# Optimization experiments

Hardware: AMD Instinct MI355X
Metric: run time of the kernel (lower is better)

Reference implementation:

```python
import jax, jax.numpy as jnp
import numpy as np
from jax import lax

V, E, H = 32000, 512, 1024  # vocab, embedding_dim, hidden_dim
S, B, T = 50, 64, 10        # src len, batch, max decode steps
SOS = 0


def setup_inputs() -> dict:
    key = jax.random.key(0)
    ks = jax.random.split(key, 16)
    sc = 0.02
    n = jax.random.normal
    return {
        "enc_out": n(ks[0], (S, B, 2 * H), jnp.float32),
        "hidden": n(ks[1], (1, B, H), jnp.float32),
        "target": jax.random.randint(ks[2], (B, T), 0, V),
        "emb": n(ks[3], (V, E), jnp.float32) * sc,
        "w_ih": n(ks[4], (3 * H, E), jnp.float32) * sc,
        "w_hh": n(ks[5], (3 * H, H), jnp.float32) * sc,
        "b_ih": n(ks[6], (3 * H,), jnp.float32) * sc,
        "b_hh": n(ks[7], (3 * H,), jnp.float32) * sc,
        "wa_w": n(ks[8], (H, H), jnp.float32) * sc,
        "wa_b": n(ks[9], (H,), jnp.float32) * sc,
        "ua_w": n(ks[10], (H, 2 * H), jnp.float32) * sc,
        "ua_b": n(ks[11], (H,), jnp.float32) * sc,
        "va_w": n(ks[12], (1, H), jnp.float32) * sc,
        "va_b": n(ks[13], (1,), jnp.float32) * sc,
    }


def reference(enc_out, hidden, target, emb, w_ih, w_hh, b_ih, b_hh,
              wa_w, wa_b, ua_w, ua_b, va_w, va_b):
    b, t = target.shape

    def gru_cell(x, h):
        gi = x @ w_ih.T + b_ih          # [B, 3H]
        gh = h @ w_hh.T + b_hh          # [B, 3H]
        ir, iz, inn = jnp.split(gi, 3, axis=-1)
        hr, hz, hn = jnp.split(gh, 3, axis=-1)
        r = jax.nn.sigmoid(ir + hr)
        z = jax.nn.sigmoid(iz + hz)
        nng = jnp.tanh(inn + r * hn)
        return (1.0 - z) * nng + z * h

    # teacher-forced decoder inputs: [SOS, target[:, :-1]] -> [T, B]
    dec_in = jnp.concatenate(
        [jnp.full((b, 1), SOS, dtype=target.dtype), target[:, : t - 1]], axis=1)
    xs = emb[dec_in].transpose(1, 0, 2)  # [T, B, E] (dropout is identity in eval)

    def step(h, x):
        h2 = gru_cell(x, h)
        return h2, h2

    h_last, hs = lax.scan(step, hidden[0], xs)   # hs: [T, B, H]

    keys = enc_out.transpose(1, 0, 2)            # [B, S, 2H]
    uk = keys @ ua_w.T + ua_b                    # [B, S, H]
    wq = hs @ wa_w.T + wa_b                      # [T, B, H]
    # additive (Bahdanau) scores: [T, B, S]
    scores = (jnp.tanh(wq[:, :, None, :] + uk[None]) @ va_w.T + va_b)[..., 0]
    weights = jax.nn.softmax(scores, axis=-1)    # over source positions
    context = jnp.einsum('tbs,bsd->btd', weights, keys)  # [B, T, 2H]
    out = jax.nn.log_softmax(context, axis=-1)   # [B, T, 2H]
    return out, h_last
```

## Files before the change

### kernel.cpp

```cpp
#include <hip/hip_runtime.h>
#include <math.h>

#define VOCAB 32000
#define E_DIM 512
#define H_DIM 1024
#define S_LEN 50
#define B_SZ 64
#define T_LEN 10
#define H3 (3 * H_DIM)
#define D2H (2 * H_DIM)

typedef __attribute__((ext_vector_type(8))) short short8;
typedef __attribute__((ext_vector_type(4))) float floatx4;

__device__ __forceinline__ ushort f2b(float f) {
    union { float f; uint32_t u; } x; x.f = f;
    uint32_t r = (x.u + 0x7fff + ((x.u >> 16) & 1)) >> 16;
    return (ushort)r;
}
__device__ __forceinline__ float b2f(ushort u) {
    union { float f; uint32_t u; } x; x.u = ((uint32_t)u) << 16;
    return x.f;
}
__device__ __forceinline__ float fast_sigmoid(float x) {
    x = fminf(fmaxf(x, -30.f), 30.f);
    return 1.f / (1.f + __expf(-x));
}
__device__ __forceinline__ float fast_tanh(float x) {
    x = fminf(fmaxf(x, -15.f), 15.f);
    float e = __expf(2.f * x);
    return (e - 1.f) / (e + 1.f);
}

#define PB0 1536
#define PB1 (PB0 + 3072)
#define PB2 (PB1 + 2048)
#define PB3 (PB2 + 1024)
#define PB4 (PB3 + 3200)
#define PB5 (PB4 + 640)
#define PB6 (PB5 + 64)

__device__ __forceinline__ void cvt_chunk(const float* src, ushort* dst, int i) {
    float4 v = ((const float4*)src)[i];
    ushort4 o;
    o.x = f2b(v.x); o.y = f2b(v.y); o.z = f2b(v.z); o.w = f2b(v.w);
    ((ushort4*)dst)[i] = o;
}

__global__ __launch_bounds__(256) void prep(
    const float* __restrict__ w_ih, ushort* __restrict__ w_ihb,
    const float* __restrict__ w_hh, ushort* __restrict__ w_hhb,
    const float* __restrict__ ua_w, ushort* __restrict__ ua_wb,
    const float* __restrict__ wa_w, ushort* __restrict__ wa_wb,
    const float* __restrict__ enc_out, ushort* __restrict__ keysb,
    const int* __restrict__ target, const float* __restrict__ emb,
    ushort* __restrict__ Xb,
    const float* __restrict__ hidden, ushort* __restrict__ hb0,
    int* __restrict__ bar) {
    int bid = blockIdx.x, tid = threadIdx.x;
    if (bid == 0) {
        for (int i = tid; i < 4096; i += 256)
            __hip_atomic_store(&bar[i], 0, __ATOMIC_RELAXED, __HIP_MEMORY_SCOPE_AGENT);
    }
    if (bid < PB0) {
        cvt_chunk(w_ih, w_ihb, bid * 256 + tid);
    } else if (bid < PB1) {
        cvt_chunk(w_hh, w_hhb, (bid - PB0) * 256 + tid);
    } else if (bid < PB2) {
        cvt_chunk(ua_w, ua_wb, (bid - PB1) * 256 + tid);
    } else if (bid < PB3) {
        cvt_chunk(wa_w, wa_wb, (bid - PB2) * 256 + tid);
    } else if (bid < PB4) {
        int bs = bid - PB3;
        int b = bs / S_LEN, s = bs % S_LEN;
        const float* src = enc_out + ((size_t)s * B_SZ + b) * D2H;
        ushort* dst = keysb + (size_t)bs * D2H;
#pragma unroll
        for (int p = 0; p < 2; ++p) {
            int i = tid + p * 256;
            float4 v = ((const float4*)src)[i];
            ushort4 o;
            o.x = f2b(v.x); o.y = f2b(v.y); o.z = f2b(v.z); o.w = f2b(v.w);
            ((ushort4*)dst)[i] = o;
        }
    } else if (bid < PB5) {
        int m = bid - PB4;
        int t = m / B_SZ, b = m % B_SZ;
        int idx = (t == 0) ? 0 : target[b * T_LEN + (t - 1)];
        if (tid < 128) {
            const float* src = emb + (size_t)idx * E_DIM;
            float4 v = ((const float4*)src)[tid];
            ushort4 o;
            o.x = f2b(v.x); o.y = f2b(v.y); o.z = f2b(v.z); o.w = f2b(v.w);
            ((ushort4*)(Xb + (size_t)m * E_DIM))[tid] = o;
        }
    } else {
        cvt_chunk(hidden, hb0, (bid - PB5) * 256 + tid);
    }
}

struct GemmArgs {
    const ushort* A; const ushort* W; const float* bias;
    float* Cf; ushort* C16;
    int M, N, K, nbn, nblk;
};

__global__ __launch_bounds__(256) void gemm_bf16(GemmArgs g0, GemmArgs g1) {
    const bool first = (int)blockIdx.x < g0.nblk;
    GemmArgs g = first ? g0 : g1;
    const int bid = first ? blockIdx.x : (blockIdx.x - g0.nblk);

    __shared__ ushort As[64 * 72];
    __shared__ ushort Bs[128 * 72];

    const int tid = threadIdx.x;
    const int w = tid >> 6, lane = tid & 63;
    const int lm = lane & 15, q = lane >> 4;
    const int wm = w >> 1, wn = w & 1;
    const int n0 = (bid % g.nbn) * 128;
    const int m0 = (bid / g.nbn) * 64;
    const int K = g.K;

    floatx4 acc[2][4];
#pragma unroll
    for (int i = 0; i < 2; ++i)
#pragma unroll
        for (int j = 0; j < 4; ++j)
            acc[i][j] = (floatx4){0.f, 0.f, 0.f, 0.f};

    short8 ar[2], br[4];
    auto load_tiles = [&](int k0) {
#pragma unroll
        for (int p = 0; p < 2; ++p) {
            int c = tid + p * 256;
            ar[p] = *(const short8*)&g.A[(size_t)(m0 + (c >> 3)) * K + k0 + (c & 7) * 8];
        }
#pragma unroll
        for (int p = 0; p < 4; ++p) {
            int c = tid + p * 256;
            br[p] = *(const short8*)&g.W[(size_t)(n0 + (c >> 3)) * K + k0 + (c & 7) * 8];
        }
    };

    load_tiles(0);
    for (int k0 = 0; k0 < K; k0 += 64) {
#pragma unroll
        for (int p = 0; p < 2; ++p) {
            int c = tid + p * 256;
            *(short8*)&As[(c >> 3) * 72 + (c & 7) * 8] = ar[p];
        }
#pragma unroll
        for (int p = 0; p < 4; ++p) {
            int c = tid + p * 256;
            *(short8*)&Bs[(c >> 3) * 72 + (c & 7) * 8] = br[p];
        }
        __syncthreads();
        if (k0 + 64 < K) load_tiles(k0 + 64);

#pragma unroll
        for (int kk = 0; kk < 2; ++kk) {
            short8 af[2], bf[4];
#pragma unroll
            for (int i = 0; i < 2; ++i)
                af[i] = *(const short8*)&As[(wm * 32 + i * 16 + lm) * 72 + kk * 32 + q * 8];
#pragma unroll
            for (int j = 0; j < 4; ++j)
                bf[j] = *(const short8*)&Bs[(wn * 64 + j * 16 + lm) * 72 + kk * 32 + q * 8];
#pragma unroll
            for (int i = 0; i < 2; ++i)
#pragma unroll
                for (int j = 0; j < 4; ++j)
                    acc[i][j] = __builtin_amdgcn_mfma_f32_16x16x32_bf16(af[i], bf[j], acc[i][j], 0, 0, 0);
        }
        __syncthreads();
    }

    float bv[4];
#pragma unroll
    for (int j = 0; j < 4; ++j)
        bv[j] = g.bias[n0 + wn * 64 + j * 16 + lm];
#pragma unroll
    for (int i = 0; i < 2; ++i) {
#pragma unroll
        for (int j = 0; j < 4; ++j) {
            int col = n0 + wn * 64 + j * 16 + lm;
#pragma unroll
            for (int r = 0; r < 4; ++r) {
                int row = m0 + wm * 32 + i * 16 + q * 4 + r;
                float v = acc[i][j][r] + bv[j];
                if (g.C16) g.C16[(size_t)row * g.N + col] = f2b(v);
                else       g.Cf[(size_t)row * g.N + col] = v;
            }
        }
    }
}

#define GRU_BLOCKS 64
#define WS_STRIDE 1032

__device__ __forceinline__ void grid_barrier(int* __restrict__ bar, int t, int bid) {
    __syncthreads();
    if (threadIdx.x == 0) {
        __builtin_amdgcn_fence(__ATOMIC_RELEASE, "agent");
        int g = bid & 7;
        int sub = __hip_atomic_fetch_add(&bar[(t * 8 + g) * 32], 1,
                                         __ATOMIC_RELAXED, __HIP_MEMORY_SCOPE_AGENT);
        if (sub == 7) {
            int m = __hip_atomic_fetch_add(&bar[2560 + t * 32], 1,
                                           __ATOMIC_RELAXED, __HIP_MEMORY_SCOPE_AGENT);
            if (m == 7)
                __hip_atomic_store(&bar[3040], t + 1,
                                   __ATOMIC_RELAXED, __HIP_MEMORY_SCOPE_AGENT);
        }
        while (__hip_atomic_load(&bar[3040], __ATOMIC_RELAXED,
                                 __HIP_MEMORY_SCOPE_AGENT) <= t)
            __builtin_amdgcn_s_sleep(1);
        __builtin_amdgcn_fence(__ATOMIC_ACQUIRE, "agent");
    }
    __syncthreads();
}

__global__ __launch_bounds__(256, 1) void gru_persistent(
    const ushort* __restrict__ w_hhb, const float* __restrict__ bhh,
    const float* __restrict__ GI, const float* __restrict__ hidden,
    const ushort* __restrict__ hb0, ushort* __restrict__ hsb,
    float* __restrict__ outTail, int* __restrict__ bar) {
    __shared__ ushort Ws[48 * WS_STRIDE];
    const int tid = threadIdx.x;
    const int w = tid >> 6, lane = tid & 63;
    const int lm = lane & 15, q = lane >> 4;
    const int bid = blockIdx.x;
    const int j0 = bid * 16;
    const int j = j0 + lm;

#pragma unroll
    for (int p = 0; p < 24; ++p) {
        int c = tid + p * 256;
        int row = c >> 7, off = c & 127;
        int grow = (row >> 4) * H_DIM + j0 + (row & 15);
        *(short8*)&Ws[row * WS_STRIDE + off * 8] =
            *(const short8*)&w_hhb[(size_t)grow * H_DIM + off * 8];
    }

    const float bhr = bhh[j], bhz = bhh[H_DIM + j], bhn = bhh[2 * H_DIM + j];

    float hf[4];
#pragma unroll
    for (int r = 0; r < 4; ++r)
        hf[r] = hidden[(size_t)(w * 16 + q * 4 + r) * H_DIM + j];

    float ir[4], iz[4], inn[4];
#pragma unroll
    for (int r = 0; r < 4; ++r) {
        const float* gi = GI + (size_t)(w * 16 + q * 4 + r) * H3 + j;
        ir[r] = gi[0]; iz[r] = gi[H_DIM]; inn[r] = gi[2 * H_DIM];
    }

    __syncthreads();

    for (int t = 0; t < T_LEN; ++t) {
        const ushort* hin = (t == 0) ? hb0 : hsb + (size_t)(t - 1) * B_SZ * H_DIM;
        ushort* hout = hsb + (size_t)t * B_SZ * H_DIM;
        const ushort* arow = hin + (size_t)(w * 16 + lm) * H_DIM + q * 8;

        short8 hreg[32];
#pragma unroll
        for (int c = 0; c < 32; ++c)
            hreg[c] = *(const short8*)&arow[c * 32];

        floatx4 accr = {0.f, 0.f, 0.f, 0.f};
        floatx4 accz = {0.f, 0.f, 0.f, 0.f};
        floatx4 accn = {0.f, 0.f, 0.f, 0.f};

#pragma unroll
        for (int it = 0; it < 8; ++it) {
#pragma unroll
            for (int kk = 0; kk < 4; ++kk) {
                const short8 af = hreg[it * 4 + kk];
                const int ko = it * 128 + kk * 32 + q * 8;
                short8 b0 = *(const short8*)&Ws[(lm) * WS_STRIDE + ko];
                short8 b1 = *(const short8*)&Ws[(16 + lm) * WS_STRIDE + ko];
                short8 b2 = *(const short8*)&Ws[(32 + lm) * WS_STRIDE + ko];
                accr = __builtin_amdgcn_mfma_f32_16x16x32_bf16(af, b0, accr, 0, 0, 0);
                accz = __builtin_amdgcn_mfma_f32_16x16x32_bf16(af, b1, accz, 0, 0, 0);
                accn = __builtin_amdgcn_mfma_f32_16x16x32_bf16(af, b2, accn, 0, 0, 0);
            }
        }

#pragma unroll
        for (int r = 0; r < 4; ++r) {
            int b = w * 16 + q * 4 + r;
            float rg = fast_sigmoid(ir[r] + accr[r] + bhr);
            float z  = fast_sigmoid(iz[r] + accz[r] + bhz);
            float ng = fast_tanh(inn[r] + rg * (accn[r] + bhn));
            float hnew = (1.f - z) * ng + z * hf[r];
            hf[r] = hnew;
            size_t hi = (size_t)b * H_DIM + j;
            hout[hi] = f2b(hnew);
            if (t == T_LEN - 1) outTail[hi] = hnew;
        }

        if (t < T_LEN - 1) {
#pragma unroll
            for (int r = 0; r < 4; ++r) {
                const float* gi = GI + (size_t)((t + 1) * B_SZ + w * 16 + q * 4 + r) * H3 + j;
                ir[r] = gi[0]; iz[r] = gi[H_DIM]; inn[r] = gi[2 * H_DIM];
            }
            grid_barrier(bar, t, bid);
        }
    }
}

__global__ __launch_bounds__(256) void attn_ctx(
    const ushort* __restrict__ WQ16, const ushort* __restrict__ UK16,
    const float* __restrict__ va_w, const float* __restrict__ va_b,
    const ushort* __restrict__ keysb, float* __restrict__ out) {
    __shared__ float wq_s[H_DIM];
    __shared__ float va_s[H_DIM];
    __shared__ float sc[S_LEN];
    __shared__ float wred[4];
    __shared__ float sred[4];
    const int bt = blockIdx.x;
    const int t = bt >> 6, b = bt & 63;
    const int tid = threadIdx.x;
    const int wave = tid >> 6, lane = tid & 63;

    for (int hh = tid; hh < H_DIM; hh += 256) {
        wq_s[hh] = b2f(WQ16[(size_t)(t * B_SZ + b) * H_DIM + hh]);
        va_s[hh] = va_w[hh];
    }
    __syncthreads();

    for (int s = wave; s < S_LEN; s += 4) {
        const ushort* uk = UK16 + ((size_t)b * S_LEN + s) * H_DIM + lane * 16;
        short8 u0 = *(const short8*)&uk[0];
        short8 u1 = *(const short8*)&uk[8];
        float acc = 0.f;
        const int h0 = lane * 16;
#pragma unroll
        for (int i = 0; i < 8; ++i)
            acc += fast_tanh(wq_s[h0 + i] + b2f((ushort)u0[i])) * va_s[h0 + i];
#pragma unroll
        for (int i = 0; i < 8; ++i)
            acc += fast_tanh(wq_s[h0 + 8 + i] + b2f((ushort)u1[i])) * va_s[h0 + 8 + i];
        for (int off = 32; off > 0; off >>= 1) acc += __shfl_down(acc, off);
        if (lane == 0) sc[s] = acc + va_b[0];
    }
    __syncthreads();

    if (tid < 64) {
        float v = (tid < S_LEN) ? sc[tid] : -INFINITY;
        float m = v;
        for (int off = 32; off > 0; off >>= 1) m = fmaxf(m, __shfl_down(m, off));
        m = __shfl(m, 0);
        float e = (tid < S_LEN) ? __expf(v - m) : 0.f;
        float sum = e;
        for (int off = 32; off > 0; off >>= 1) sum += __shfl_down(sum, off);
        sum = __shfl(sum, 0);
        if (tid < S_LEN) sc[tid] = e / sum;
    }
    __syncthreads();

    float c[8];
#pragma unroll
    for (int i = 0; i < 8; ++i) c[i] = 0.f;
    const ushort* kb = keysb + (size_t)b * S_LEN * D2H + tid * 8;
    for (int s = 0; s < S_LEN; ++s) {
        float ws = sc[s];
        short8 kv = *(const short8*)&kb[(size_t)s * D2H];
#pragma unroll
        for (int i = 0; i < 8; ++i) c[i] += ws * b2f((ushort)kv[i]);
    }

    float m = c[0];
#pragma unroll
    for (int i = 1; i < 8; ++i) m = fmaxf(m, c[i]);
    for (int off = 32; off > 0; off >>= 1) m = fmaxf(m, __shfl_down(m, off));
    if (lane == 0) wred[wave] = m;
    __syncthreads();
    if (tid == 0) wred[0] = fmaxf(fmaxf(wred[0], wred[1]), fmaxf(wred[2], wred[3]));
    __syncthreads();
    m = wred[0];
    float sum = 0.f;
#pragma unroll
    for (int i = 0; i < 8; ++i) sum += __expf(c[i] - m);
    for (int off = 32; off > 0; off >>= 1) sum += __shfl_down(sum, off);
    if (lane == 0) sred[wave] = sum;
    __syncthreads();
    if (tid == 0) sred[0] = sred[0] + sred[1] + sred[2] + sred[3];
    __syncthreads();
    float lse = m + __logf(sred[0]);

    float* o = out + ((size_t)b * T_LEN + t) * D2H + tid * 8;
#pragma unroll
    for (int i = 0; i < 8; ++i) o[i] = c[i] - lse;
}

extern "C" void kernel_launch(void* const* d_in, const int* in_sizes, int n_in,
                              void* d_out, int out_size, void* d_ws, size_t ws_size,
                              hipStream_t stream) {
    const float* enc_out = (const float*)d_in[0];
    const float* hidden  = (const float*)d_in[1];
    const int*   target  = (const int*)d_in[2];
    const float* emb     = (const float*)d_in[3];
    const float* w_ih    = (const float*)d_in[4];
    const float* w_hh    = (const float*)d_in[5];
    const float* b_ih    = (const float*)d_in[6];
    const float* b_hh    = (const float*)d_in[7];
    const float* wa_w    = (const float*)d_in[8];
    const float* wa_b    = (const float*)d_in[9];
    const float* ua_w    = (const float*)d_in[10];
    const float* ua_b    = (const float*)d_in[11];
    const float* va_w    = (const float*)d_in[12];
    const float* va_b    = (const float*)d_in[13];
    float* out = (float*)d_out;

    const int TB = T_LEN * B_SZ;
    const int BS = B_SZ * S_LEN;

    char* p = (char*)d_ws;
    int*    bar   = (int*)p;    p += 4096 * 4;
    float*  GI    = (float*)p;  p += (size_t)TB * H3 * 4;
    p = (char*)(((uintptr_t)p + 255) & ~(uintptr_t)255);
    ushort* keysb = (ushort*)p; p += (size_t)BS * D2H * 2;
    ushort* Xb    = (ushort*)p; p += (size_t)TB * E_DIM * 2;
    ushort* w_ihb = (ushort*)p; p += (size_t)H3 * E_DIM * 2;
    ushort* w_hhb = (ushort*)p; p += (size_t)H3 * H_DIM * 2;
    ushort* ua_wb = (ushort*)p; p += (size_t)H_DIM * D2H * 2;
    ushort* wa_wb = (ushort*)p; p += (size_t)H_DIM * H_DIM * 2;
    ushort* hb0   = (ushort*)p; p += (size_t)B_SZ * H_DIM * 2;
    ushort* hsb   = (ushort*)p; p += (size_t)TB * H_DIM * 2;
    ushort* UK16  = (ushort*)p; p += (size_t)BS * H_DIM * 2;
    ushort* WQ16  = (ushort*)p; p += (size_t)TB * H_DIM * 2;

    prep<<<PB6, 256, 0, stream>>>(w_ih, w_ihb, w_hh, w_hhb, ua_w, ua_wb, wa_w, wa_wb,
                                  enc_out, keysb, target, emb, Xb, hidden, hb0, bar);

    GemmArgs guk = { keysb, ua_wb, ua_b, nullptr, UK16,
                     BS, H_DIM, D2H, H_DIM / 128, (BS / 64) * (H_DIM / 128) };
    GemmArgs ggi = { Xb, w_ihb, b_ih, GI, nullptr,
                     TB, H3, E_DIM, H3 / 128, (TB / 64) * (H3 / 128) };
    gemm_bf16<<<guk.nblk + ggi.nblk, 256, 0, stream>>>(guk, ggi);

    float* outTail = out + (size_t)B_SZ * T_LEN * D2H;
    gru_persistent<<<GRU_BLOCKS, 256, 0, stream>>>(w_hhb, b_hh, GI, hidden,
                                                   hb0, hsb, outTail, bar);

    GemmArgs gwq = { hsb, wa_wb, wa_b, nullptr, WQ16,
                     TB, H_DIM, H_DIM, H_DIM / 128, (TB / 64) * (H_DIM / 128) };
    gemm_bf16<<<gwq.nblk, 256, 0, stream>>>(gwq, gwq);

    attn_ctx<<<B_SZ * T_LEN, 256, 0, stream>>>(WQ16, UK16, va_w, va_b, keysb, out);
}
```

Baseline: 332.9 us.

## Replace grid-barrier fences with system-scope atomics and cache-bypassing hidden-state loads

Measured after the change: 309.2 us. -7.1%, faster.

```diff
diff --git a/kernel.cpp b/kernel.cpp
--- a/kernel.cpp
+++ b/kernel.cpp
@@ -60,7 +60,7 @@
     int bid = blockIdx.x, tid = threadIdx.x;
     if (bid == 0) {
         for (int i = tid; i < 4096; i += 256)
-            __hip_atomic_store(&bar[i], 0, __ATOMIC_RELAXED, __HIP_MEMORY_SCOPE_AGENT);
+            __hip_atomic_store(&bar[i], 0, __ATOMIC_RELAXED, __HIP_MEMORY_SCOPE_SYSTEM);
     }
     if (bid < PB0) {
         cvt_chunk(w_ih, w_ihb, bid * 256 + tid);
@@ -201,21 +201,19 @@
 __device__ __forceinline__ void grid_barrier(int* __restrict__ bar, int t, int bid) {
     __syncthreads();
     if (threadIdx.x == 0) {
-        __builtin_amdgcn_fence(__ATOMIC_RELEASE, "agent");
         int g = bid & 7;
         int sub = __hip_atomic_fetch_add(&bar[(t * 8 + g) * 32], 1,
-                                         __ATOMIC_RELAXED, __HIP_MEMORY_SCOPE_AGENT);
+                                         __ATOMIC_RELAXED, __HIP_MEMORY_SCOPE_SYSTEM);
         if (sub == 7) {
             int m = __hip_atomic_fetch_add(&bar[2560 + t * 32], 1,
-                                           __ATOMIC_RELAXED, __HIP_MEMORY_SCOPE_AGENT);
+                                           __ATOMIC_RELAXED, __HIP_MEMORY_SCOPE_SYSTEM);
             if (m == 7)
                 __hip_atomic_store(&bar[3040], t + 1,
-                                   __ATOMIC_RELAXED, __HIP_MEMORY_SCOPE_AGENT);
+                                   __ATOMIC_RELAXED, __HIP_MEMORY_SCOPE_SYSTEM);
         }
         while (__hip_atomic_load(&bar[3040], __ATOMIC_RELAXED,
-                                 __HIP_MEMORY_SCOPE_AGENT) <= t)
+                                 __HIP_MEMORY_SCOPE_SYSTEM) <= t)
             __builtin_amdgcn_s_sleep(1);
-        __builtin_amdgcn_fence(__ATOMIC_ACQUIRE, "agent");
     }
     __syncthreads();
 }
@@ -263,10 +261,51 @@
         ushort* hout = hsb + (size_t)t * B_SZ * H_DIM;
         const ushort* arow = hin + (size_t)(w * 16 + lm) * H_DIM + q * 8;
 
-        short8 hreg[32];
-#pragma unroll
-        for (int c = 0; c < 32; ++c)
-            hreg[c] = *(const short8*)&arow[c * 32];
+        short8 hr[32];
+        asm volatile(
+            "global_load_dwordx4 %[h0], %[a], off sc0 sc1\n\t"
+            "global_load_dwordx4 %[h1], %[a], off offset:64 sc0 sc1\n\t"
+            "global_load_dwordx4 %[h2], %[a], off offset:128 sc0 sc1\n\t"
+            "global_load_dwordx4 %[h3], %[a], off offset:192 sc0 sc1\n\t"
+            "global_load_dwordx4 %[h4], %[a], off offset:256 sc0 sc1\n\t"
+            "global_load_dwordx4 %[h5], %[a], off offset:320 sc0 sc1\n\t"
+            "global_load_dwordx4 %[h6], %[a], off offset:384 sc0 sc1\n\t"
+            "global_load_dwordx4 %[h7], %[a], off offset:448 sc0 sc1\n\t"
+            "global_load_dwordx4 %[h8], %[a], off offset:512 sc0 sc1\n\t"
+            "global_load_dwordx4 %[h9], %[a], off offset:576 sc0 sc1\n\t"
+            "global_load_dwordx4 %[h10], %[a], off offset:640 sc0 sc1\n\t"
+            "global_load_dwordx4 %[h11], %[a], off offset:704 sc0 sc1\n\t"
+            "global_load_dwordx4 %[h12], %[a], off offset:768 sc0 sc1\n\t"
+            "global_load_dwordx4 %[h13], %[a], off offset:832 sc0 sc1\n\t"
+            "global_load_dwordx4 %[h14], %[a], off offset:896 sc0 sc1\n\t"
+            "global_load_dwordx4 %[h15], %[a], off offset:960 sc0 sc1\n\t"
+            "global_load_dwordx4 %[h16], %[a], off offset:1024 sc0 sc1\n\t"
+            "global_load_dwordx4 %[h17], %[a], off offset:1088 sc0 sc1\n\t"
+            "global_load_dwordx4 %[h18], %[a], off offset:1152 sc0 sc1\n\t"
+            "global_load_dwordx4 %[h19], %[a], off offset:1216 sc0 sc1\n\t"
+            "global_load_dwordx4 %[h20], %[a], off offset:1280 sc0 sc1\n\t"
+            "global_load_dwordx4 %[h21], %[a], off offset:1344 sc0 sc1\n\t"
+            "global_load_dwordx4 %[h22], %[a], off offset:1408 sc0 sc1\n\t"
+            "global_load_dwordx4 %[h23], %[a], off offset:1472 sc0 sc1\n\t"
+            "global_load_dwordx4 %[h24], %[a], off offset:1536 sc0 sc1\n\t"
+            "global_load_dwordx4 %[h25], %[a], off offset:1600 sc0 sc1\n\t"
+            "global_load_dwordx4 %[h26], %[a], off offset:1664 sc0 sc1\n\t"
+            "global_load_dwordx4 %[h27], %[a], off offset:1728 sc0 sc1\n\t"
+            "global_load_dwordx4 %[h28], %[a], off offset:1792 sc0 sc1\n\t"
+            "global_load_dwordx4 %[h29], %[a], off offset:1856 sc0 sc1\n\t"
+            "global_load_dwordx4 %[h30], %[a], off offset:1920 sc0 sc1\n\t"
+            "global_load_dwordx4 %[h31], %[a], off offset:1984 sc0 sc1\n\t"
+            "s_waitcnt vmcnt(0)"
+            : [h0] "=&v"(hr[0]), [h1] "=&v"(hr[1]), [h2] "=&v"(hr[2]), [h3] "=&v"(hr[3]),
+              [h4] "=&v"(hr[4]), [h5] "=&v"(hr[5]), [h6] "=&v"(hr[6]), [h7] "=&v"(hr[7]),
+              [h8] "=&v"(hr[8]), [h9] "=&v"(hr[9]), [h10] "=&v"(hr[10]), [h11] "=&v"(hr[11]),
+              [h12] "=&v"(hr[12]), [h13] "=&v"(hr[13]), [h14] "=&v"(hr[14]), [h15] "=&v"(hr[15]),
+              [h16] "=&v"(hr[16]), [h17] "=&v"(hr[17]), [h18] "=&v"(hr[18]), [h19] "=&v"(hr[19]),
+              [h20] "=&v"(hr[20]), [h21] "=&v"(hr[21]), [h22] "=&v"(hr[22]), [h23] "=&v"(hr[23]),
+              [h24] "=&v"(hr[24]), [h25] "=&v"(hr[25]), [h26] "=&v"(hr[26]), [h27] "=&v"(hr[27]),
+              [h28] "=&v"(hr[28]), [h29] "=&v"(hr[29]), [h30] "=&v"(hr[30]), [h31] "=&v"(hr[31])
+            : [a] "v"(arow)
+            : "memory");
 
         floatx4 accr = {0.f, 0.f, 0.f, 0.f};
         floatx4 accz = {0.f, 0.f, 0.f, 0.f};
@@ -276,7 +315,7 @@
         for (int it = 0; it < 8; ++it) {
 #pragma unroll
             for (int kk = 0; kk < 4; ++kk) {
-                const short8 af = hreg[it * 4 + kk];
+                const short8 af = hr[it * 4 + kk];
                 const int ko = it * 128 + kk * 32 + q * 8;
                 short8 b0 = *(const short8*)&Ws[(lm) * WS_STRIDE + ko];
                 short8 b1 = *(const short8*)&Ws[(16 + lm) * WS_STRIDE + ko];
@@ -287,17 +326,29 @@
             }
         }
 
+        int h16v[4];
 #pragma unroll
         for (int r = 0; r < 4; ++r) {
-            int b = w * 16 + q * 4 + r;
             float rg = fast_sigmoid(ir[r] + accr[r] + bhr);
             float z  = fast_sigmoid(iz[r] + accz[r] + bhz);
             float ng = fast_tanh(inn[r] + rg * (accn[r] + bhn));
             float hnew = (1.f - z) * ng + z * hf[r];
             hf[r] = hnew;
-            size_t hi = (size_t)b * H_DIM + j;
-            hout[hi] = f2b(hnew);
-            if (t == T_LEN - 1) outTail[hi] = hnew;
+            h16v[r] = (int)f2b(hnew);
+            if (t == T_LEN - 1) {
+                int b = w * 16 + q * 4 + r;
+                outTail[(size_t)b * H_DIM + j] = hnew;
+            }
+        }
+#pragma unroll
+        for (int r = 0; r < 4; ++r) {
+            int pv = __shfl(h16v[r], (lane + 1) & 63);
+            if ((lm & 1) == 0) {
+                int b = w * 16 + q * 4 + r;
+                uint packed = (uint)(h16v[r] & 0xffff) | ((uint)pv << 16);
+                __hip_atomic_store((uint*)hout + ((size_t)b * H_DIM + j) / 2, packed,
+                                   __ATOMIC_RELAXED, __HIP_MEMORY_SCOPE_SYSTEM);
+            }
         }
 
         if (t < T_LEN - 1) {
```
